# Kernel optimization log

Measured on AMD Instinct MI355X. Metric: run time of the kernel, lower is better.

Reference implementation:

```python
import jax, jax.numpy as jnp
import numpy as np

DIST_THRES = 0.2
EPS = 1e-8


def _project(points, extrinsic, intrinsic):
    # points: [N,3] world; extrinsic: cam-to-world [4,4]; intrinsic: normalized [3,3]
    w2c = jnp.linalg.inv(extrinsic)
    hom = jnp.concatenate([points, jnp.ones_like(points[:, :1])], axis=-1)  # [N,4]
    cam = hom @ w2c.T  # [N,4]
    z = cam[:, 2]
    valid_z = z > EPS
    xy = cam[:, :2] / jnp.maximum(z, EPS)[:, None]
    ndc = xy @ intrinsic[:2, :2].T + intrinsic[:2, 2]  # [N,2] in [0,1] if visible
    return ndc, valid_z


def _remove_redundancy_batch(means_v, covs_v, shs_v, opas_v, scales_v, rots_v, extr, intr, h, w):
    # means_v: [v,hw,3]; extr: [v,4,4]; intr: [v,3,3]
    v, hw = means_v.shape[0], means_v.shape[1]
    n_total = v * hw
    attrs = (means_v, covs_v, shs_v, opas_v, scales_v, rots_v)

    def init_buf(x):
        buf = jnp.zeros((n_total,) + x.shape[2:], x.dtype)
        return buf.at[:hw].set(x[0])  # view 0 kept wholesale

    bufs = [init_buf(a) for a in attrs]
    valid = jnp.zeros((n_total,), bool).at[:hw].set(True)

    for view in range(1, v):  # small fixed view count: python loop ok
        ndc, vz = _project(bufs[0], extr[view], intr[view])
        m = (ndc[:, 0] >= 0) & (ndc[:, 0] < 1) & (ndc[:, 1] >= 0) & (ndc[:, 1] < 1) & vz & valid
        x = jnp.floor(ndc[:, 0] * w).astype(jnp.int32)
        y = jnp.floor(ndc[:, 1] * h).astype(jnp.int32)
        # original indexes with stride h (y*h + x); bug-faithful, requires h == w
        pix = jnp.clip(y * h + x, 0, hw - 1)
        vpts = means_v[view][pix]  # gather candidate view gaussian at projected pixel
        dist = jnp.linalg.norm(bufs[0] - vpts, axis=1)
        occ = m & (dist <= DIST_THRES)  # accumulated gaussians that cover a pixel of this view
        idx = jnp.where(occ, pix, hw)  # dump masked-out entries into overflow slot
        keep = jnp.ones((hw + 1,), bool).at[idx].set(False)[:hw]  # unoccupied pixels -> keep new gaussian
        sl = slice(view * hw, (view + 1) * hw)
        new_vals = tuple(a[view] for a in attrs)
        bufs = [b.at[sl].set(jnp.where(keep.reshape((-1,) + (1,) * (nv.ndim - 1)), nv, 0))
                for b, nv in zip(bufs, new_vals)]
        valid = valid.at[sl].set(keep)
    return bufs + [valid]


def reference(means, covariances, harmonics, opacities, scales, rotations, extrinsics, intrinsics, h, w):
    b = means.shape[0]
    outs = [
        _remove_redundancy_batch(means[i], covariances[i], harmonics[i], opacities[i],
                                 scales[i], rotations[i], extrinsics[i], intrinsics[i], h, w)
        for i in range(b)
    ]
    # (means, covariances, harmonics, opacities, scales, rotations, valid_mask)
    return tuple(jnp.stack([o[k] for o in outs]) for k in range(7))


def setup_inputs() -> dict:
    key = jax.random.key(0)
    b, v, h, w, d_sh = 1, 4, 256, 256, 25
    hw = h * w
    ks = jax.random.split(key, 7)
    xy = jax.random.uniform(ks[0], (b, v, hw, 2), minval=-1.5, maxval=1.5)
    z = jax.random.uniform(ks[1], (b, v, hw, 1), minval=1.0, maxval=3.0)
    means = jnp.concatenate([xy, z], axis=-1)
    covariances = jax.random.normal(ks[2], (b, v, hw, 3, 3)) * 0.01
    harmonics = jax.random.normal(ks[3], (b, v, hw, 3, d_sh))
    opacities = jax.random.uniform(ks[4], (b, v, hw))
    scales = jax.random.uniform(ks[5], (b, v, hw, 3)) * 0.05
    rotations = jax.random.normal(ks[6], (b, v, hw, 4))
    # near-identity cam-to-world with small x offsets per view
    offs = jnp.arange(v, dtype=jnp.float32) * 0.15 - 0.225
    extrinsics = jnp.tile(jnp.eye(4, dtype=jnp.float32), (b, v, 1, 1)).at[:, :, 0, 3].set(offs[None, :])
    intrinsics = (jnp.zeros((b, v, 3, 3), jnp.float32)
                  .at[:, :, 0, 0].set(1.0).at[:, :, 1, 1].set(1.0)
                  .at[:, :, 0, 2].set(0.5).at[:, :, 1, 2].set(0.5)
                  .at[:, :, 2, 2].set(1.0))
    return {"means": means, "covariances": covariances, "harmonics": harmonics,
            "opacities": opacities, "scales": scales, "rotations": rotations,
            "extrinsics": extrinsics, "intrinsics": intrinsics, "h": h, "w": w}
```

## Files before the change

kernel.cpp:

```cpp
#include <hip/hip_runtime.h>
#include <stdint.h>


__device__ void inv4x4(const float* M, float* out) {
    double m[16];
    for (int i = 0; i < 16; ++i) m[i] = (double)M[i];
    double inv[16];
    inv[0]  =  m[5]*m[10]*m[15] - m[5]*m[11]*m[14] - m[9]*m[6]*m[15] + m[9]*m[7]*m[14] + m[13]*m[6]*m[11] - m[13]*m[7]*m[10];
    inv[4]  = -m[4]*m[10]*m[15] + m[4]*m[11]*m[14] + m[8]*m[6]*m[15] - m[8]*m[7]*m[14] - m[12]*m[6]*m[11] + m[12]*m[7]*m[10];
    inv[8]  =  m[4]*m[9]*m[15]  - m[4]*m[11]*m[13] - m[8]*m[5]*m[15] + m[8]*m[7]*m[13] + m[12]*m[5]*m[11] - m[12]*m[7]*m[9];
    inv[12] = -m[4]*m[9]*m[14]  + m[4]*m[10]*m[13] + m[8]*m[5]*m[14] - m[8]*m[6]*m[13] - m[12]*m[5]*m[10] + m[12]*m[6]*m[9];
    inv[1]  = -m[1]*m[10]*m[15] + m[1]*m[11]*m[14] + m[9]*m[2]*m[15] - m[9]*m[3]*m[14] - m[13]*m[2]*m[11] + m[13]*m[3]*m[10];
    inv[5]  =  m[0]*m[10]*m[15] - m[0]*m[11]*m[14] - m[8]*m[2]*m[15] + m[8]*m[3]*m[14] + m[12]*m[2]*m[11] - m[12]*m[3]*m[10];
    inv[9]  = -m[0]*m[9]*m[15]  + m[0]*m[11]*m[13] + m[8]*m[1]*m[15] - m[8]*m[3]*m[13] - m[12]*m[1]*m[11] + m[12]*m[3]*m[9];
    inv[13] =  m[0]*m[9]*m[14]  - m[0]*m[10]*m[13] - m[8]*m[1]*m[14] + m[8]*m[2]*m[13] + m[12]*m[1]*m[10] - m[12]*m[2]*m[9];
    inv[2]  =  m[1]*m[6]*m[15]  - m[1]*m[7]*m[14]  - m[5]*m[2]*m[15] + m[5]*m[3]*m[14] + m[13]*m[2]*m[7]  - m[13]*m[3]*m[6];
    inv[6]  = -m[0]*m[6]*m[15]  + m[0]*m[7]*m[14]  + m[4]*m[2]*m[15] - m[4]*m[3]*m[14] - m[12]*m[2]*m[7]  + m[12]*m[3]*m[6];
    inv[10] =  m[0]*m[5]*m[15]  - m[0]*m[7]*m[13]  - m[4]*m[1]*m[15] + m[4]*m[3]*m[13] + m[12]*m[1]*m[7]  - m[12]*m[3]*m[5];
    inv[14] = -m[0]*m[5]*m[14]  + m[0]*m[6]*m[13]  + m[4]*m[1]*m[14] - m[4]*m[2]*m[13] - m[12]*m[1]*m[6]  + m[12]*m[2]*m[5];
    inv[3]  = -m[1]*m[6]*m[11]  + m[1]*m[7]*m[10]  + m[5]*m[2]*m[11] - m[5]*m[3]*m[10] - m[9]*m[2]*m[7]   + m[9]*m[3]*m[6];
    inv[7]  =  m[0]*m[6]*m[11]  - m[0]*m[7]*m[10]  - m[4]*m[2]*m[11] + m[4]*m[3]*m[10] + m[8]*m[2]*m[7]   - m[8]*m[3]*m[6];
    inv[11] = -m[0]*m[5]*m[11]  + m[0]*m[7]*m[9]   + m[4]*m[1]*m[11] - m[4]*m[3]*m[9]  - m[8]*m[1]*m[7]   + m[8]*m[3]*m[5];
    inv[15] =  m[0]*m[5]*m[10]  - m[0]*m[6]*m[9]   - m[4]*m[1]*m[10] + m[4]*m[2]*m[9]  + m[8]*m[1]*m[6]   - m[8]*m[2]*m[5];
    double det = m[0]*inv[0] + m[1]*inv[4] + m[2]*inv[8] + m[3]*inv[12];
    double idet = 1.0 / det;
    for (int i = 0; i < 16; ++i) out[i] = (float)(inv[i] * idet);
}

__global__ void init_kernel(const float* __restrict__ extr, float* __restrict__ w2c,
                            uint32_t* __restrict__ bitmap_words, int v, int n_words) {
    int tid = blockIdx.x * blockDim.x + threadIdx.x;
    int stride = gridDim.x * blockDim.x;
    for (int i = tid; i < n_words; i += stride) bitmap_words[i] = 0u;
    if (tid < v) inv4x4(extr + tid * 16, w2c + tid * 16);
}

__global__ void mark_kernel(const float* __restrict__ means_all,
                            const uint8_t* __restrict__ bm_all,
                            const float* __restrict__ means_view,
                            const float* __restrict__ w2c,
                            const float* __restrict__ intr,
                            uint8_t* __restrict__ bitmap_out,
                            int n_prev, const int* __restrict__ hp,
                            const int* __restrict__ wp, int hw) {
#pragma clang fp contract(off)
    int i = blockIdx.x * blockDim.x + threadIdx.x;
    if (i >= n_prev) return;
    if (bm_all[i] != 0) return;
    float px = means_all[3 * i + 0];
    float py = means_all[3 * i + 1];
    float pz = means_all[3 * i + 2];
    float c0 = w2c[0] * px + w2c[1] * py + w2c[2]  * pz + w2c[3];
    float c1 = w2c[4] * px + w2c[5] * py + w2c[6]  * pz + w2c[7];
    float c2 = w2c[8] * px + w2c[9] * py + w2c[10] * pz + w2c[11];
    bool vz = c2 > 1e-8f;
    float zz = fmaxf(c2, 1e-8f);
    float xp = c0 / zz;
    float yp = c1 / zz;
    float n0 = (xp * intr[0] + yp * intr[1]) + intr[2];
    float n1 = (xp * intr[3] + yp * intr[4]) + intr[5];
    bool m = (n0 >= 0.0f) & (n0 < 1.0f) & (n1 >= 0.0f) & (n1 < 1.0f) & vz;
    if (!m) return;
    int w_ = *wp;
    int h_ = *hp;
    int x = (int)floorf(n0 * (float)w_);
    int y = (int)floorf(n1 * (float)h_);
    int pix = y * h_ + x;
    pix = min(max(pix, 0), hw - 1);
    float vx = means_view[3 * pix + 0];
    float vy = means_view[3 * pix + 1];
    float vw = means_view[3 * pix + 2];
    float dx = px - vx, dy = py - vy, dz = pz - vw;
    float dist = sqrtf((dx * dx + dy * dy) + dz * dz);
    if (dist <= 0.2f) bitmap_out[pix] = 1;
}

__global__ void __launch_bounds__(256) write_all(
        const float4* __restrict__ means, const float4* __restrict__ covs,
        const float4* __restrict__ shs,   const float4* __restrict__ opas,
        const float4* __restrict__ scales,const float4* __restrict__ rots,
        const uint8_t* __restrict__ bm,   float4* __restrict__ out, long N) {
    const long N4 = N >> 2;
    const long B0 = 3 * N4, B1 = 12 * N4, B2 = 87 * N4, B3 = 88 * N4,
               B4 = 91 * N4, B5 = 95 * N4, B6 = 96 * N4;
    long q = (long)blockIdx.x * blockDim.x + threadIdx.x;
    if (q >= B6) return;
    float4 v;
    if (q < B0) {
        long t = q, e = 4 * t;
        v = means[t];
        if (bm[(e + 0) / 3]) v.x = 0.f;
        if (bm[(e + 1) / 3]) v.y = 0.f;
        if (bm[(e + 2) / 3]) v.z = 0.f;
        if (bm[(e + 3) / 3]) v.w = 0.f;
    } else if (q < B1) {
        long t = q - B0, e = 4 * t;
        v = covs[t];
        if (bm[(e + 0) / 9]) v.x = 0.f;
        if (bm[(e + 1) / 9]) v.y = 0.f;
        if (bm[(e + 2) / 9]) v.z = 0.f;
        if (bm[(e + 3) / 9]) v.w = 0.f;
    } else if (q < B2) {
        long t = q - B1, e = 4 * t;
        v = shs[t];
        if (bm[(e + 0) / 75]) v.x = 0.f;
        if (bm[(e + 1) / 75]) v.y = 0.f;
        if (bm[(e + 2) / 75]) v.z = 0.f;
        if (bm[(e + 3) / 75]) v.w = 0.f;
    } else if (q < B3) {
        long t = q - B2, e = 4 * t;
        v = opas[t];
        if (bm[e + 0]) v.x = 0.f;
        if (bm[e + 1]) v.y = 0.f;
        if (bm[e + 2]) v.z = 0.f;
        if (bm[e + 3]) v.w = 0.f;
    } else if (q < B4) {
        long t = q - B3, e = 4 * t;
        v = scales[t];
        if (bm[(e + 0) / 3]) v.x = 0.f;
        if (bm[(e + 1) / 3]) v.y = 0.f;
        if (bm[(e + 2) / 3]) v.z = 0.f;
        if (bm[(e + 3) / 3]) v.w = 0.f;
    } else if (q < B5) {
        long t = q - B4;
        v = rots[t];
        if (bm[t]) v = make_float4(0.f, 0.f, 0.f, 0.f);
    } else {
        long t = q - B5, e = 4 * t;
        v.x = bm[e + 0] ? 0.f : 1.f;
        v.y = bm[e + 1] ? 0.f : 1.f;
        v.z = bm[e + 2] ? 0.f : 1.f;
        v.w = bm[e + 3] ? 0.f : 1.f;
    }
    out[q] = v;
}

extern "C" void kernel_launch(void* const* d_in, const int* in_sizes, int n_in,
                              void* d_out, int out_size, void* d_ws, size_t ws_size,
                              hipStream_t stream) {
    const float* means  = (const float*)d_in[0];
    const float* covs   = (const float*)d_in[1];
    const float* shs    = (const float*)d_in[2];
    const float* opas   = (const float*)d_in[3];
    const float* scales = (const float*)d_in[4];
    const float* rots   = (const float*)d_in[5];
    const float* extr   = (const float*)d_in[6];
    const float* intr   = (const float*)d_in[7];
    const int*   hp     = (const int*)d_in[8];
    const int*   wp     = (const int*)d_in[9];

    const int v  = in_sizes[6] / 16;
    const int hw = in_sizes[3] / v;
    const long N = (long)v * hw;

    float*   w2c     = (float*)d_ws;
    uint8_t* bitmaps = (uint8_t*)d_ws + 1024;

    {
        int n_words = (int)(N / 4);
        int blocks = (n_words + 255) / 256;
        init_kernel<<<blocks, 256, 0, stream>>>(extr, w2c, (uint32_t*)bitmaps, v, n_words);
    }

    for (int view = 1; view < v; ++view) {
        int n_prev = view * hw;
        int mblocks = (n_prev + 255) / 256;
        mark_kernel<<<mblocks, 256, 0, stream>>>(means, bitmaps,
                                                 means + (long)view * hw * 3,
                                                 w2c + view * 16, intr + view * 9,
                                                 bitmaps + (long)view * hw,
                                                 n_prev, hp, wp, hw);
    }

    const long n4 = 96L * (N >> 2);
    const int wblocks = (int)((n4 + 255) / 256);
    write_all<<<wblocks, 256, 0, stream>>>((const float4*)means, (const float4*)covs,
                                           (const float4*)shs, (const float4*)opas,
                                           (const float4*)scales, (const float4*)rots,
                                           bitmaps, (float4*)d_out, N);
}
```

Measured before the change: 201.1 us.

## Fuse init, per-view marking, and output write into one cooperative persistent kernel

Replaces the init kernel, the per-view mark kernel launches and the final write kernel with a single cooperative kernel. It uses grid-stride loops and grid.sync() between phases. This removes several kernel launches and their gaps. In exchange it uses a grid of only blocksPerCU*256 blocks, which may cut memory parallelism in the large streaming write phase, and it adds grid-wide barrier costs.

Result: slower. 497.6 us (+147.4%).

```diff
diff --git a/kernel.cpp b/kernel.cpp
--- a/kernel.cpp
+++ b/kernel.cpp
@@ -1,5 +1,8 @@
 #include <hip/hip_runtime.h>
+#include <hip/hip_cooperative_groups.h>
 #include <stdint.h>
+
+namespace cg = cooperative_groups;
 
 
 __device__ void inv4x4(const float* M, float* out) {
@@ -27,112 +30,132 @@
     for (int i = 0; i < 16; ++i) out[i] = (float)(inv[i] * idet);
 }
 
-__global__ void init_kernel(const float* __restrict__ extr, float* __restrict__ w2c,
-                            uint32_t* __restrict__ bitmap_words, int v, int n_words) {
-    int tid = blockIdx.x * blockDim.x + threadIdx.x;
-    int stride = gridDim.x * blockDim.x;
-    for (int i = tid; i < n_words; i += stride) bitmap_words[i] = 0u;
-    if (tid < v) inv4x4(extr + tid * 16, w2c + tid * 16);
-}
+__global__ void __launch_bounds__(256, 4) fused_cascade(
+        const float* __restrict__ means, const float* __restrict__ covs,
+        const float* __restrict__ shs,   const float* __restrict__ opas,
+        const float* __restrict__ scales,const float* __restrict__ rots,
+        const float* __restrict__ extr,  const float* __restrict__ intr,
+        const int* __restrict__ hp, const int* __restrict__ wp,
+        float* __restrict__ out, float* __restrict__ w2c_g,
+        uint8_t* __restrict__ bitmaps, int nv, int hw) {
+#pragma clang fp contract(off)
+    cg::grid_group grid = cg::this_grid();
+    const long N = (long)nv * hw;
+    const int tid = blockIdx.x * blockDim.x + threadIdx.x;
+    const int nthreads = gridDim.x * blockDim.x;
 
-__global__ void mark_kernel(const float* __restrict__ means_all,
-                            const uint8_t* __restrict__ bm_all,
-                            const float* __restrict__ means_view,
-                            const float* __restrict__ w2c,
-                            const float* __restrict__ intr,
-                            uint8_t* __restrict__ bitmap_out,
-                            int n_prev, const int* __restrict__ hp,
-                            const int* __restrict__ wp, int hw) {
-#pragma clang fp contract(off)
-    int i = blockIdx.x * blockDim.x + threadIdx.x;
-    if (i >= n_prev) return;
-    if (bm_all[i] != 0) return;
-    float px = means_all[3 * i + 0];
-    float py = means_all[3 * i + 1];
-    float pz = means_all[3 * i + 2];
-    float c0 = w2c[0] * px + w2c[1] * py + w2c[2]  * pz + w2c[3];
-    float c1 = w2c[4] * px + w2c[5] * py + w2c[6]  * pz + w2c[7];
-    float c2 = w2c[8] * px + w2c[9] * py + w2c[10] * pz + w2c[11];
-    bool vz = c2 > 1e-8f;
-    float zz = fmaxf(c2, 1e-8f);
-    float xp = c0 / zz;
-    float yp = c1 / zz;
-    float n0 = (xp * intr[0] + yp * intr[1]) + intr[2];
-    float n1 = (xp * intr[3] + yp * intr[4]) + intr[5];
-    bool m = (n0 >= 0.0f) & (n0 < 1.0f) & (n1 >= 0.0f) & (n1 < 1.0f) & vz;
-    if (!m) return;
-    int w_ = *wp;
-    int h_ = *hp;
-    int x = (int)floorf(n0 * (float)w_);
-    int y = (int)floorf(n1 * (float)h_);
-    int pix = y * h_ + x;
-    pix = min(max(pix, 0), hw - 1);
-    float vx = means_view[3 * pix + 0];
-    float vy = means_view[3 * pix + 1];
-    float vw = means_view[3 * pix + 2];
-    float dx = px - vx, dy = py - vy, dz = pz - vw;
-    float dist = sqrtf((dx * dx + dy * dy) + dz * dz);
-    if (dist <= 0.2f) bitmap_out[pix] = 1;
-}
+    {
+        uint32_t* bw = (uint32_t*)bitmaps;
+        int n_words = (int)(N >> 2);
+        for (int i = tid; i < n_words; i += nthreads) bw[i] = 0u;
+        if (tid < nv) inv4x4(extr + tid * 16, w2c_g + tid * 16);
+    }
+    grid.sync();
 
-__global__ void __launch_bounds__(256) write_all(
-        const float4* __restrict__ means, const float4* __restrict__ covs,
-        const float4* __restrict__ shs,   const float4* __restrict__ opas,
-        const float4* __restrict__ scales,const float4* __restrict__ rots,
-        const uint8_t* __restrict__ bm,   float4* __restrict__ out, long N) {
-    const long N4 = N >> 2;
-    const long B0 = 3 * N4, B1 = 12 * N4, B2 = 87 * N4, B3 = 88 * N4,
-               B4 = 91 * N4, B5 = 95 * N4, B6 = 96 * N4;
-    long q = (long)blockIdx.x * blockDim.x + threadIdx.x;
-    if (q >= B6) return;
-    float4 v;
-    if (q < B0) {
-        long t = q, e = 4 * t;
-        v = means[t];
-        if (bm[(e + 0) / 3]) v.x = 0.f;
-        if (bm[(e + 1) / 3]) v.y = 0.f;
-        if (bm[(e + 2) / 3]) v.z = 0.f;
-        if (bm[(e + 3) / 3]) v.w = 0.f;
-    } else if (q < B1) {
-        long t = q - B0, e = 4 * t;
-        v = covs[t];
-        if (bm[(e + 0) / 9]) v.x = 0.f;
-        if (bm[(e + 1) / 9]) v.y = 0.f;
-        if (bm[(e + 2) / 9]) v.z = 0.f;
-        if (bm[(e + 3) / 9]) v.w = 0.f;
-    } else if (q < B2) {
-        long t = q - B1, e = 4 * t;
-        v = shs[t];
-        if (bm[(e + 0) / 75]) v.x = 0.f;
-        if (bm[(e + 1) / 75]) v.y = 0.f;
-        if (bm[(e + 2) / 75]) v.z = 0.f;
-        if (bm[(e + 3) / 75]) v.w = 0.f;
-    } else if (q < B3) {
-        long t = q - B2, e = 4 * t;
-        v = opas[t];
-        if (bm[e + 0]) v.x = 0.f;
-        if (bm[e + 1]) v.y = 0.f;
-        if (bm[e + 2]) v.z = 0.f;
-        if (bm[e + 3]) v.w = 0.f;
-    } else if (q < B4) {
-        long t = q - B3, e = 4 * t;
-        v = scales[t];
-        if (bm[(e + 0) / 3]) v.x = 0.f;
-        if (bm[(e + 1) / 3]) v.y = 0.f;
-        if (bm[(e + 2) / 3]) v.z = 0.f;
-        if (bm[(e + 3) / 3]) v.w = 0.f;
-    } else if (q < B5) {
-        long t = q - B4;
-        v = rots[t];
-        if (bm[t]) v = make_float4(0.f, 0.f, 0.f, 0.f);
-    } else {
-        long t = q - B5, e = 4 * t;
-        v.x = bm[e + 0] ? 0.f : 1.f;
-        v.y = bm[e + 1] ? 0.f : 1.f;
-        v.z = bm[e + 2] ? 0.f : 1.f;
-        v.w = bm[e + 3] ? 0.f : 1.f;
+    const int w_ = *wp;
+    const int h_ = *hp;
+    for (int view = 1; view < nv; ++view) {
+        const int n_prev = view * hw;
+        const float* mv = means + (long)view * hw * 3;
+        const float* W  = w2c_g + view * 16;
+        const float* K  = intr + view * 9;
+        uint8_t* bmo    = bitmaps + (long)view * hw;
+        float W0=W[0],W1=W[1],W2=W[2],W3=W[3],W4=W[4],W5=W[5],W6=W[6],W7=W[7],
+              W8=W[8],W9=W[9],W10=W[10],W11=W[11];
+        float K0=K[0],K1=K[1],K2=K[2],K3=K[3],K4=K[4],K5=K[5];
+        for (int i = tid; i < n_prev; i += nthreads) {
+            if (bitmaps[i] != 0) continue;
+            float px = means[3 * i + 0];
+            float py = means[3 * i + 1];
+            float pz = means[3 * i + 2];
+            float c0 = W0 * px + W1 * py + W2  * pz + W3;
+            float c1 = W4 * px + W5 * py + W6  * pz + W7;
+            float c2 = W8 * px + W9 * py + W10 * pz + W11;
+            bool vz = c2 > 1e-8f;
+            float zz = fmaxf(c2, 1e-8f);
+            float xp = c0 / zz;
+            float yp = c1 / zz;
+            float n0 = (xp * K0 + yp * K1) + K2;
+            float n1 = (xp * K3 + yp * K4) + K5;
+            bool m = (n0 >= 0.0f) & (n0 < 1.0f) & (n1 >= 0.0f) & (n1 < 1.0f) & vz;
+            if (!m) continue;
+            int x = (int)floorf(n0 * (float)w_);
+            int y = (int)floorf(n1 * (float)h_);
+            int pix = y * h_ + x;
+            pix = min(max(pix, 0), hw - 1);
+            float vx = mv[3 * pix + 0];
+            float vy = mv[3 * pix + 1];
+            float vw = mv[3 * pix + 2];
+            float dx = px - vx, dy = py - vy, dz = pz - vw;
+            float dist = sqrtf((dx * dx + dy * dy) + dz * dz);
+            if (dist <= 0.2f) bmo[pix] = 1;
+        }
+        grid.sync();
     }
-    out[q] = v;
+
+    {
+        const long N4 = N >> 2;
+        const long B0 = 3 * N4, B1 = 12 * N4, B2 = 87 * N4, B3 = 88 * N4,
+                   B4 = 91 * N4, B5 = 95 * N4, B6 = 96 * N4;
+        const float4* m4 = (const float4*)means;
+        const float4* c4 = (const float4*)covs;
+        const float4* s4 = (const float4*)shs;
+        const float4* o4 = (const float4*)opas;
+        const float4* l4 = (const float4*)scales;
+        const float4* r4 = (const float4*)rots;
+        const uint8_t* bm = bitmaps;
+        float4* out4 = (float4*)out;
+        for (long q = tid; q < B6; q += nthreads) {
+            float4 val;
+            if (q < B0) {
+                long t = q, e = 4 * t;
+                val = m4[t];
+                if (bm[(e + 0) / 3]) val.x = 0.f;
+                if (bm[(e + 1) / 3]) val.y = 0.f;
+                if (bm[(e + 2) / 3]) val.z = 0.f;
+                if (bm[(e + 3) / 3]) val.w = 0.f;
+            } else if (q < B1) {
+                long t = q - B0, e = 4 * t;
+                val = c4[t];
+                if (bm[(e + 0) / 9]) val.x = 0.f;
+                if (bm[(e + 1) / 9]) val.y = 0.f;
+                if (bm[(e + 2) / 9]) val.z = 0.f;
+                if (bm[(e + 3) / 9]) val.w = 0.f;
+            } else if (q < B2) {
+                long t = q - B1, e = 4 * t;
+                val = s4[t];
+                if (bm[(e + 0) / 75]) val.x = 0.f;
+                if (bm[(e + 1) / 75]) val.y = 0.f;
+                if (bm[(e + 2) / 75]) val.z = 0.f;
+                if (bm[(e + 3) / 75]) val.w = 0.f;
+            } else if (q < B3) {
+                long t = q - B2, e = 4 * t;
+                val = o4[t];
+                if (bm[e + 0]) val.x = 0.f;
+                if (bm[e + 1]) val.y = 0.f;
+                if (bm[e + 2]) val.z = 0.f;
+                if (bm[e + 3]) val.w = 0.f;
+            } else if (q < B4) {
+                long t = q - B3, e = 4 * t;
+                val = l4[t];
+                if (bm[(e + 0) / 3]) val.x = 0.f;
+                if (bm[(e + 1) / 3]) val.y = 0.f;
+                if (bm[(e + 2) / 3]) val.z = 0.f;
+                if (bm[(e + 3) / 3]) val.w = 0.f;
+            } else if (q < B5) {
+                long t = q - B4;
+                val = r4[t];
+                if (bm[t]) val = make_float4(0.f, 0.f, 0.f, 0.f);
+            } else {
+                long t = q - B5, e = 4 * t;
+                val.x = bm[e + 0] ? 0.f : 1.f;
+                val.y = bm[e + 1] ? 0.f : 1.f;
+                val.z = bm[e + 2] ? 0.f : 1.f;
+                val.w = bm[e + 3] ? 0.f : 1.f;
+            }
+            out4[q] = val;
+        }
+    }
 }
 
 extern "C" void kernel_launch(void* const* d_in, const int* in_sizes, int n_in,
@@ -149,33 +172,23 @@
     const int*   hp     = (const int*)d_in[8];
     const int*   wp     = (const int*)d_in[9];
 
-    const int v  = in_sizes[6] / 16;
-    const int hw = in_sizes[3] / v;
-    const long N = (long)v * hw;
+    int nv = in_sizes[6] / 16;
+    int hw = in_sizes[3] / nv;
 
     float*   w2c     = (float*)d_ws;
     uint8_t* bitmaps = (uint8_t*)d_ws + 1024;
+    float*   out     = (float*)d_out;
 
-    {
-        int n_words = (int)(N / 4);
-        int blocks = (n_words + 255) / 256;
-        init_kernel<<<blocks, 256, 0, stream>>>(extr, w2c, (uint32_t*)bitmaps, v, n_words);
-    }
+    int blocksPerCU = 0;
+    if (hipOccupancyMaxActiveBlocksPerMultiprocessor(&blocksPerCU,
+            (const void*)fused_cascade, 256, 0) != hipSuccess || blocksPerCU <= 0)
+        blocksPerCU = 4;
+    int grid = blocksPerCU * 256;
 
-    for (int view = 1; view < v; ++view) {
-        int n_prev = view * hw;
-        int mblocks = (n_prev + 255) / 256;
-        mark_kernel<<<mblocks, 256, 0, stream>>>(means, bitmaps,
-                                                 means + (long)view * hw * 3,
-                                                 w2c + view * 16, intr + view * 9,
-                                                 bitmaps + (long)view * hw,
-                                                 n_prev, hp, wp, hw);
-    }
-
-    const long n4 = 96L * (N >> 2);
-    const int wblocks = (int)((n4 + 255) / 256);
-    write_all<<<wblocks, 256, 0, stream>>>((const float4*)means, (const float4*)covs,
-                                           (const float4*)shs, (const float4*)opas,
-                                           (const float4*)scales, (const float4*)rots,
-                                           bitmaps, (float4*)d_out, N);
+    void* args[] = { (void*)&means, (void*)&covs, (void*)&shs, (void*)&opas,
+                     (void*)&scales, (void*)&rots, (void*)&extr, (void*)&intr,
+                     (void*)&hp, (void*)&wp, (void*)&out, (void*)&w2c,
+                     (void*)&bitmaps, (void*)&nv, (void*)&hw };
+    hipLaunchCooperativeKernel((void*)fused_cascade, dim3(grid), dim3(256),
+                               args, 0, stream);
 }
```
